# Kernel optimization log

Measured on AMD Instinct MI355X. Metric: run time of the kernel, lower is better.

Reference implementation:

```python
import jax, jax.numpy as jnp
import numpy as np

# Mex config (matches init_kwargs)
B, C, H, W = 64, 64, 64, 64
BLK = (64, 3, 3)        # block over (C, H, W); spans all channels -> out_c = 1
STR = (64, 2, 2)
PAD = (0, 1, 1)
NI = 256                # num_instances
EPS = 1.0
SOFTMAX_MODE = False    # False -> mean (logsumexp - log k), True -> plain logsumexp


def setup_inputs() -> dict:
    key = jax.random.key(0)
    k1, k2 = jax.random.split(key)
    x = jax.random.normal(k1, (B, C, H, W), dtype=jnp.float32)
    kblk = BLK[0] * BLK[1] * BLK[2]
    # Dirichlet([1]*k) init == normalized exponentials; nregions = 1 (shared offsets)
    e = jax.random.exponential(k2, (1, NI, kblk), dtype=jnp.float32)
    offsets = (e / jnp.sum(e, axis=-1, keepdims=True)).reshape(1, NI, *BLK)
    return {"x": x, "offsets": offsets}


def _mex_forward(x, offsets):
    eps = jnp.float32(EPS)
    bc, bh, bw = BLK
    # im2col patch extraction: (B, C*bh*bw, OH, OW); feature dim ordered (c, fh, fw)
    patches = jax.lax.conv_general_dilated_patches(
        x, (bh, bw), (STR[1], STR[2]),
        [(PAD[1], PAD[1]), (PAD[2], PAD[2])],  # zero padding == blocks_out_of_bounds_value
        dimension_numbers=("NCHW", "OIHW", "NCHW"),
    )
    Bn, K, OH, OW = patches.shape  # K = bc*bh*bw = 576
    P = patches.transpose(0, 2, 3, 1).reshape(-1, K)  # (N, k), N = B*OH*OW
    O = offsets.reshape(NI, K)                         # single shared region

    # y_ni = (1/eps) * logsumexp_k( eps*(P_nk + O_ik) ) - log(k)/eps (mean mode)
    # exp-domain GEMM with max-shift for stability:
    Pe = eps * P
    Oe = eps * O
    mp = jnp.max(Pe, axis=1, keepdims=True)   # (N, 1)
    mo = jnp.max(Oe, axis=1, keepdims=True)   # (I, 1)
    S = jnp.exp(Pe - mp) @ jnp.exp(Oe - mo).T  # (N, I)
    y = (jnp.log(S) + mp + mo.T) / eps
    if not SOFTMAX_MODE:
        y = y - jnp.log(jnp.float32(K)) / eps
    # output: (B, num_instances * out_c, OH, OW) with out_c = 1
    return y.reshape(Bn, OH, OW, NI).transpose(0, 3, 1, 2)


def reference(x, offsets):
    return _mex_forward(x, offsets)
```

## Files before the change

### kernel.cpp

```cpp
#include <hip/hip_runtime.h>
#include <hip/hip_bf16.h>


typedef __bf16 bf16x8 __attribute__((ext_vector_type(8)));
typedef float  f32x4  __attribute__((ext_vector_type(4)));

__global__ void mex_prep_b(const float* __restrict__ off, __bf16* __restrict__ Bt) {
    const int i = blockIdx.x * 4 + (threadIdx.x >> 6);
    const int c = threadIdx.x & 63;
    const float* oi = off + i * 576;
    __bf16* bi = Bt + i * 576;
    #pragma unroll
    for (int p = 0; p < 9; ++p) {
        float v = oi[c * 9 + p];
        bi[p * 64 + c] = (__bf16)__expf(v);
    }
}

__global__ __launch_bounds__(256, 3) void mex_main(
        const float* __restrict__ x,
        const __bf16* __restrict__ Bt,
        float* __restrict__ out) {
    __shared__ bf16x8 lds8[5 * 66 * 8];

    const int bid = blockIdx.x;
    const int b   = bid >> 4;
    const int oh0 = (bid & 15) << 1;
    const int tid  = threadIdx.x;
    const int wv   = tid >> 6;

    bf16x8 one8;
    #pragma unroll
    for (int j = 0; j < 8; ++j) one8[j] = (__bf16)1.0f;
    if (tid < 40) {
        const int hl = tid >> 3, cc = tid & 7;
        lds8[(hl * 66) * 8 + cc] = one8;
    }
    if (oh0 == 0) {
        for (int i = tid; i < 66 * 8; i += 256) lds8[i] = one8;
    }

    {
        const int wp  = tid & 31;
        const int w0  = wp << 1;
        const int c8  = tid >> 5;
        const int c8p = c8 ^ (wp & 7);
        const float* xb = x + ((size_t)b << 18) + w0;
        #pragma unroll
        for (int hl = 0; hl < 5; ++hl) {
            const int hg = 2 * oh0 - 1 + hl;
            if (hg >= 0) {
                const float* xp = xb + (hg << 6);
                float2 v[8];
                #pragma unroll
                for (int k = 0; k < 8; ++k)
                    v[k] = *(const float2*)(xp + (((c8 << 3) + k) << 12));
                bf16x8 ca, cb;
                #pragma unroll
                for (int k = 0; k < 8; ++k) {
                    ca[k] = (__bf16)__expf(v[k].x);
                    cb[k] = (__bf16)__expf(v[k].y);
                }
                bf16x8* dst = lds8 + hl * 528 + (w0 + 1) * 8 + c8p;
                dst[0] = ca;
                dst[8] = cb;
            }
        }
    }
    __syncthreads();

    const int t16 = tid & 15;
    const int q   = (tid >> 4) & 3;

    int rbase[4], owv[4];
    #pragma unroll
    for (int mt = 0; mt < 4; ++mt) {
        const int m = mt * 16 + t16;
        owv[mt]   = m & 31;
        rbase[mt] = ((m >> 5) * 132) + ((m & 31) * 2);
    }

    const bf16x8* __restrict__ Btv = (const bf16x8*)Bt;
    const int instRow = (wv * 64 + t16) * 72 + q;

    f32x4 acc[4][4];
    #pragma unroll
    for (int mt = 0; mt < 4; ++mt)
        #pragma unroll
        for (int nt = 0; nt < 4; ++nt)
            acc[mt][nt] = (f32x4)(0.0f);

    bf16x8 bcur[4];
    #pragma unroll
    for (int nt = 0; nt < 4; ++nt)
        bcur[nt] = Btv[instRow + nt * (16 * 72)];

    #pragma unroll 2
    for (int ks = 0; ks < 18; ++ks) {
        const int p  = ks >> 1;
        const int fh = (p * 11) >> 5;
        const int fw = p - fh * 3;
        const int rofs = fh * 66 + fw;
        const int ccq  = ((ks & 1) << 2) + q;

        bf16x8 a[4];
        #pragma unroll
        for (int mt = 0; mt < 4; ++mt) {
            const int row = rbase[mt] + rofs;
            const int key = ((owv[mt] * 2 + fw - 1) >> 1) & 7;
            a[mt] = lds8[row * 8 + (ccq ^ key)];
        }

        bf16x8 bnext[4];
        if (ks < 17) {
            #pragma unroll
            for (int nt = 0; nt < 4; ++nt)
                bnext[nt] = Btv[instRow + nt * (16 * 72) + (ks + 1) * 4];
        }

        #pragma unroll
        for (int mt = 0; mt < 4; ++mt)
            #pragma unroll
            for (int nt = 0; nt < 4; ++nt)
                acc[mt][nt] = __builtin_amdgcn_mfma_f32_16x16x32_bf16(
                    a[mt], bcur[nt], acc[mt][nt], 0, 0, 0);

        #pragma unroll
        for (int nt = 0; nt < 4; ++nt) bcur[nt] = bnext[nt];
    }

    const float lK = 6.356107660695891f;
    #pragma unroll
    for (int mt = 0; mt < 4; ++mt) {
        const int m   = mt * 16 + (q << 2);
        const int ohl = m >> 5;
        const int owi = m & 31;
        const int orow = (oh0 + ohl) * 32 + owi;
        #pragma unroll
        for (int nt = 0; nt < 4; ++nt) {
            const int inst = wv * 64 + nt * 16 + t16;
            f32x4 r;
            #pragma unroll
            for (int j = 0; j < 4; ++j)
                r[j] = __logf(acc[mt][nt][j]) - lK;
            *(f32x4*)(out + (((size_t)b * 256 + inst) * 1024 + orow)) = r;
        }
    }
}

extern "C" void kernel_launch(void* const* d_in, const int* in_sizes, int n_in,
                              void* d_out, int out_size, void* d_ws, size_t ws_size,
                              hipStream_t stream) {
    const float* x   = (const float*)d_in[0];
    const float* off = (const float*)d_in[1];
    float* out = (float*)d_out;
    __bf16* Bt = (__bf16*)d_ws;

    mex_prep_b<<<64, 256, 0, stream>>>(off, Bt);
    mex_main<<<1024, 256, 0, stream>>>(x, Bt, out);
}
```

Before: 155.9 us.

## Pre-swizzle B fragments for coalesced loads, shrink LDS, raise occupancy

The prep kernel now writes exp(offsets) in the exact per-lane MFMA fragment order, so each wave loads B with contiguous 16-byte-per-lane accesses instead of strided rows. The LDS tile drops its left padding column; out-of-bounds columns are handled in registers by selecting a ones vector, and the first B prefetch is moved before the barrier. The loop is fully unrolled and launch bounds are raised to 4 blocks per SIMD, trading register headroom for occupancy. This risks register spills and adds per-access select logic.

Measured after the change: 152.1 us. 1.03x faster.

```diff
diff --git a/kernel.cpp b/kernel.cpp
--- a/kernel.cpp
+++ b/kernel.cpp
@@ -8,36 +8,39 @@
 __global__ void mex_prep_b(const float* __restrict__ off, __bf16* __restrict__ Bt) {
     const int i = blockIdx.x * 4 + (threadIdx.x >> 6);
     const int c = threadIdx.x & 63;
+    const int c8 = c >> 3, j = c & 7;
+    const int wv = i >> 6, nt = (i >> 4) & 3, t16 = i & 15;
+    const int q  = c8 & 3;
     const float* oi = off + i * 576;
-    __bf16* bi = Bt + i * 576;
     #pragma unroll
     for (int p = 0; p < 9; ++p) {
         float v = oi[c * 9 + p];
-        bi[p * 64 + c] = (__bf16)__expf(v);
+        const int ks    = p * 2 + (c8 >> 2);
+        const int chunk = (ks * 16 + wv * 4 + nt) * 64 + q * 16 + t16;
+        Bt[chunk * 8 + j] = (__bf16)__expf(v);
     }
 }
 
-__global__ __launch_bounds__(256, 3) void mex_main(
+__global__ __launch_bounds__(256, 4) void mex_main(
         const float* __restrict__ x,
         const __bf16* __restrict__ Bt,
         float* __restrict__ out) {
-    __shared__ bf16x8 lds8[5 * 66 * 8];
+    __shared__ bf16x8 lds8[5 * 64 * 8];
 
     const int bid = blockIdx.x;
     const int b   = bid >> 4;
     const int oh0 = (bid & 15) << 1;
     const int tid  = threadIdx.x;
     const int wv   = tid >> 6;
+    const int lane = tid & 63;
 
     bf16x8 one8;
     #pragma unroll
     for (int j = 0; j < 8; ++j) one8[j] = (__bf16)1.0f;
-    if (tid < 40) {
-        const int hl = tid >> 3, cc = tid & 7;
-        lds8[(hl * 66) * 8 + cc] = one8;
-    }
+
     if (oh0 == 0) {
-        for (int i = tid; i < 66 * 8; i += 256) lds8[i] = one8;
+        #pragma unroll
+        for (int i = 0; i < 2; ++i) lds8[tid + i * 256] = one8;
     }
 
     {
@@ -61,27 +64,32 @@
                     ca[k] = (__bf16)__expf(v[k].x);
                     cb[k] = (__bf16)__expf(v[k].y);
                 }
-                bf16x8* dst = lds8 + hl * 528 + (w0 + 1) * 8 + c8p;
+                bf16x8* dst = lds8 + hl * 512 + w0 * 8 + c8p;
                 dst[0] = ca;
                 dst[8] = cb;
             }
         }
     }
+
+    const bf16x8* __restrict__ Btv = (const bf16x8*)Bt;
+    const int wv4 = wv << 2;
+    bf16x8 bcur[4];
+    #pragma unroll
+    for (int nt = 0; nt < 4; ++nt)
+        bcur[nt] = Btv[(wv4 + nt) * 64 + lane];
+
     __syncthreads();
 
     const int t16 = tid & 15;
     const int q   = (tid >> 4) & 3;
 
-    int rbase[4], owv[4];
+    int hb[4], wo2[4];
     #pragma unroll
     for (int mt = 0; mt < 4; ++mt) {
         const int m = mt * 16 + t16;
-        owv[mt]   = m & 31;
-        rbase[mt] = ((m >> 5) * 132) + ((m & 31) * 2);
+        wo2[mt] = (m & 31) << 1;
+        hb[mt]  = (m >> 5) << 7;
     }
-
-    const bf16x8* __restrict__ Btv = (const bf16x8*)Bt;
-    const int instRow = (wv * 64 + t16) * 72 + q;
 
     f32x4 acc[4][4];
     #pragma unroll
@@ -90,32 +98,29 @@
         for (int nt = 0; nt < 4; ++nt)
             acc[mt][nt] = (f32x4)(0.0f);
 
-    bf16x8 bcur[4];
     #pragma unroll
-    for (int nt = 0; nt < 4; ++nt)
-        bcur[nt] = Btv[instRow + nt * (16 * 72)];
-
-    #pragma unroll 2
     for (int ks = 0; ks < 18; ++ks) {
         const int p  = ks >> 1;
         const int fh = (p * 11) >> 5;
         const int fw = p - fh * 3;
-        const int rofs = fh * 66 + fw;
-        const int ccq  = ((ks & 1) << 2) + q;
+        const int ccq = ((ks & 1) << 2) + q;
 
         bf16x8 a[4];
         #pragma unroll
         for (int mt = 0; mt < 4; ++mt) {
-            const int row = rbase[mt] + rofs;
-            const int key = ((owv[mt] * 2 + fw - 1) >> 1) & 7;
-            a[mt] = lds8[row * 8 + (ccq ^ key)];
+            const int wc  = wo2[mt] + fw - 1;
+            const int pad = wc < 0;
+            const int wcl = pad ? 0 : wc;
+            const int row = hb[mt] + fh * 64 + wcl;
+            bf16x8 vv = lds8[row * 8 + (ccq ^ ((wcl >> 1) & 7))];
+            a[mt] = pad ? one8 : vv;
         }
 
         bf16x8 bnext[4];
         if (ks < 17) {
             #pragma unroll
             for (int nt = 0; nt < 4; ++nt)
-                bnext[nt] = Btv[instRow + nt * (16 * 72) + (ks + 1) * 4];
+                bnext[nt] = Btv[((ks + 1) * 16 + wv4 + nt) * 64 + lane];
         }
 
         #pragma unroll
```
